# Performance work log

Measured on AMD Instinct MI355X. Metric: run time of the kernel, lower is better.

Reference implementation:

```python
import jax, jax.numpy as jnp
import numpy as np

N, DZ, L, H, MLPH, INC = 256, 256, 256, 512, 2048, 8
CAT_IDX = np.arange(0, 192, 2)                      # 96 categorical token positions (interleaved)
NUM_IDX = np.setdiff1d(np.arange(L), CAT_IDX)       # 160 numerical token positions
CARDS = [4, 16, 128]                                # cardinality per categorical group
GSZ = 32                                            # tokens per categorical group
NUM_CARD = 100                                      # cardinality of quantized numerical params


def setup_inputs() -> dict:
    ks = list(jax.random.split(jax.random.key(0), 24))
    def nrm(shape, s=0.02):
        return jax.random.normal(ks.pop(), shape, jnp.float32) * s
    inp = {}
    inp['z'] = jax.random.normal(ks.pop(), (N, DZ), jnp.float32)
    inp['mlp_w0'] = nrm((DZ, MLPH)); inp['mlp_b0'] = jnp.zeros((MLPH,), jnp.float32)
    inp['mlp_w1'] = nrm((MLPH, MLPH)); inp['mlp_b1'] = jnp.zeros((MLPH,), jnp.float32)
    inp['mlp_w2'] = nrm((MLPH, MLPH)); inp['mlp_b2'] = jnp.zeros((MLPH,), jnp.float32)
    inp['conv_w'] = nrm((H, INC)); inp['conv_b'] = jnp.zeros((H,), jnp.float32)
    for g, card in enumerate(CARDS):
        inp[f'cat_w{g}'] = nrm((H, card)); inp[f'cat_b{g}'] = jnp.zeros((card,), jnp.float32)
    inp['num_w'] = nrm((H, 2)); inp['num_b'] = jnp.zeros((2,), jnp.float32)
    inp['num_target'] = jax.random.uniform(ks.pop(), (N, len(NUM_IDX)), jnp.float32)
    inp['cat_target'] = jax.random.randint(ks.pop(), (N, len(CAT_IDX)), 0, 4, jnp.int32)
    return inp


def reference(z, mlp_w0, mlp_b0, mlp_w1, mlp_b1, mlp_w2, mlp_b2, conv_w, conv_b,
              cat_w0, cat_b0, cat_w1, cat_b1, cat_w2, cat_b2, num_w, num_b,
              num_target, cat_target):
    n = z.shape[0]
    # MLP: fc0 -> act -> fc1 -> act -> fc2
    h = z @ mlp_w0 + mlp_b0
    h = jax.nn.relu(h) @ mlp_w1 + mlp_b1
    h = jax.nn.relu(h) @ mlp_w2 + mlp_b2
    h = h.reshape(n, INC, L)                        # (N, C=8, L)
    # act + 1x1 conv to hidden_size, then transpose -> (N, L, H)
    u = jnp.einsum('ncl,hc->nlh', jax.nn.relu(h), conv_w) + conv_b
    # ---- categorical tokens: gather, per-cardinality heads, CE NLL, argmax sample ----
    hc = u[:, CAT_IDX, :]                           # (N, 96, H)
    heads = [(cat_w0, cat_b0), (cat_w1, cat_b1), (cat_w2, cat_b2)]
    nlls, samps = [], []
    for g, (w, b) in enumerate(heads):
        hg = hc[:, g * GSZ:(g + 1) * GSZ, :]        # (N, 32, H)
        logits = hg @ w + b                         # (N, 32, card)
        logp = jax.nn.log_softmax(logits, axis=-1)
        tg = cat_target[:, g * GSZ:(g + 1) * GSZ]
        nlls.append(-jnp.take_along_axis(logp, tg[..., None], axis=-1)[..., 0])
        samps.append(jnp.argmax(logits, axis=-1))
    cat_nll = jnp.concatenate(nlls, axis=1)         # (N, 96)
    cat_samples = jnp.concatenate(samps, axis=1)    # (N, 96)
    # ---- numerical tokens: gather, 2-param discretized logistic, NLL, mode sample ----
    hn = u[:, NUM_IDX, :]                           # (N, 160, H)
    p = hn @ num_w + num_b                          # (N, 160, 2)
    mu = jax.nn.sigmoid(p[..., 0])
    s = jax.nn.softplus(p[..., 1]) + 1e-4
    hb = 1.0 / (2.0 * (NUM_CARD - 1))               # half bin width
    t = num_target
    cdf_p = jax.nn.sigmoid((t + hb - mu) / s)
    cdf_m = jax.nn.sigmoid((t - hb - mu) / s)
    prob = jnp.where(t < hb, cdf_p, jnp.where(t > 1.0 - hb, 1.0 - cdf_m, cdf_p - cdf_m))
    num_nll = -jnp.log(jnp.maximum(prob, 1e-7))     # (N, 160)
    num_samples = jax.lax.stop_gradient(jnp.round(mu * (NUM_CARD - 1)) / (NUM_CARD - 1))
    # ---- scatter samples back into the preallocated output tensor ----
    u_out = jnp.zeros((n, L, 3), jnp.float32)
    u_out = u_out.at[:, CAT_IDX, 0].set(cat_samples.astype(jnp.float32))
    u_out = u_out.at[:, NUM_IDX, 1].set(num_samples)
    return u_out, cat_nll, num_nll
```

## Files before the change

### kernel.cpp

```cpp
#include <hip/hip_runtime.h>
#include <hip/hip_fp16.h>
#include <math.h>

#define NN   256
#define LL   256
#define HH   512
#define MLPHv 2048
#define INCv 8
#define NCOLS 150

typedef _Float16 f16x8 __attribute__((ext_vector_type(8)));
typedef float    f32x4 __attribute__((ext_vector_type(4)));
typedef unsigned short ushort_t;

__device__ __forceinline__ void split1(float f, ushort_t& h, ushort_t& l)
{
    __half hh = __float2half_rn(f);
    h = __half_as_ushort(hh);
    l = __half_as_ushort(__float2half_rn((f - __half2float(hh)) * 4096.f));
}

typedef __attribute__((address_space(3))) unsigned int lds_u32;
typedef __attribute__((address_space(1))) const unsigned int glb_u32;
__device__ __forceinline__ void gl_lds16(const ushort_t* g, ushort_t* l)
{
    __builtin_amdgcn_global_load_lds((glb_u32*)g, (lds_u32*)l, 16, 0, 0);
}


__global__ __launch_bounds__(256) void prep_all(
    const float* __restrict__ z,
    const float* __restrict__ w0, const float* __restrict__ w1,
    const float* __restrict__ w2,
    const float* __restrict__ cvw, const float* __restrict__ cvb,
    const float* __restrict__ cw0, const float* __restrict__ cb0,
    const float* __restrict__ cw1, const float* __restrict__ cb1,
    const float* __restrict__ cw2, const float* __restrict__ cb2,
    const float* __restrict__ nw,  const float* __restrict__ nbv,
    ushort_t* __restrict__ W0th, ushort_t* __restrict__ W0tl,
    ushort_t* __restrict__ W1th, ushort_t* __restrict__ W1tl,
    ushort_t* __restrict__ W2th, ushort_t* __restrict__ W2tl,
    ushort_t* __restrict__ zh, ushort_t* __restrict__ zl,
    float* __restrict__ Mf, float* __restrict__ beta)
{
    const int bid = blockIdx.x;
    const int tid = threadIdx.x;
    if (bid < 2176) {
        __shared__ ushort_t lh[64 * 65];
        __shared__ ushort_t ll[64 * 65];
        const float* src; ushort_t* dh; ushort_t* dl; int KS32v, t;
        if (bid < 1024)      { src = w1; dh = W1th; dl = W1tl; KS32v = 64; t = bid; }
        else if (bid < 2048) { src = w2; dh = W2th; dl = W2tl; KS32v = 64; t = bid - 1024; }
        else                 { src = w0; dh = W0th; dl = W0tl; KS32v = 8;  t = bid - 2048; }
        const int k0 = (t >> 5) * 64;
        const int n0 = (t & 31) * 64;
        {
            const int r  = tid >> 2;
            const int cb = (tid & 3) * 16;
            const float* p = src + (size_t)(k0 + r) * 2048 + n0 + cb;
            float fv[16];
#pragma unroll
            for (int q = 0; q < 4; ++q) {
                float4 v = *(const float4*)(p + q * 4);
                fv[q * 4 + 0] = v.x; fv[q * 4 + 1] = v.y;
                fv[q * 4 + 2] = v.z; fv[q * 4 + 3] = v.w;
            }
#pragma unroll
            for (int j = 0; j < 16; ++j) {
                ushort_t h, l;
                split1(fv[j], h, l);
                lh[r * 65 + cb + j] = h;
                ll[r * 65 + cb + j] = l;
            }
        }
        __syncthreads();
        {
            const int c  = tid >> 2;
            const int kq = tid & 3;
            ushort_t hb[16], lb[16];
#pragma unroll
            for (int j = 0; j < 16; ++j) {
                hb[j] = lh[(kq * 16 + j) * 65 + c];
                lb[j] = ll[(kq * 16 + j) * 65 + c];
            }
            const int gn  = (n0 + c) >> 4;
            const int l16 = c & 15;
#pragma unroll
            for (int o = 0; o < 2; ++o) {
                const int koct  = (k0 >> 3) + kq * 2 + o;
                const int ks    = koct >> 2, koct3 = koct & 3;
                const size_t off = ((size_t)(gn * KS32v + ks) * 64 + l16 + (koct3 << 4)) * 8;
                uint4 v;
                v.x = (unsigned)hb[o*8+0] | ((unsigned)hb[o*8+1] << 16);
                v.y = (unsigned)hb[o*8+2] | ((unsigned)hb[o*8+3] << 16);
                v.z = (unsigned)hb[o*8+4] | ((unsigned)hb[o*8+5] << 16);
                v.w = (unsigned)hb[o*8+6] | ((unsigned)hb[o*8+7] << 16);
                *(uint4*)&dh[off] = v;
                v.x = (unsigned)lb[o*8+0] | ((unsigned)lb[o*8+1] << 16);
                v.y = (unsigned)lb[o*8+2] | ((unsigned)lb[o*8+3] << 16);
                v.z = (unsigned)lb[o*8+4] | ((unsigned)lb[o*8+5] << 16);
                v.w = (unsigned)lb[o*8+6] | ((unsigned)lb[o*8+7] << 16);
                *(uint4*)&dl[off] = v;
            }
        }
    } else if (bid < 2192) {
        const int idx = (bid - 2176) * 256 + tid;
        const int r = idx >> 4, kq = idx & 15;
        const float* p = z + (size_t)r * 256 + kq * 16;
        float fv[16];
#pragma unroll
        for (int q = 0; q < 4; ++q) {
            float4 v = *(const float4*)(p + q * 4);
            fv[q * 4 + 0] = v.x; fv[q * 4 + 1] = v.y;
            fv[q * 4 + 2] = v.z; fv[q * 4 + 3] = v.w;
        }
        ushort_t hb[16], lb[16];
#pragma unroll
        for (int j = 0; j < 16; ++j) split1(fv[j], hb[j], lb[j]);
        const int gm = r >> 4, l16 = r & 15;
#pragma unroll
        for (int o = 0; o < 2; ++o) {
            const int koct = kq * 2 + o;
            const int ks = koct >> 2, koct3 = koct & 3;
            const size_t off = ((size_t)(gm * 8 + ks) * 64 + l16 + (koct3 << 4)) * 8;
            uint4 v;
            v.x = (unsigned)hb[o*8+0] | ((unsigned)hb[o*8+1] << 16);
            v.y = (unsigned)hb[o*8+2] | ((unsigned)hb[o*8+3] << 16);
            v.z = (unsigned)hb[o*8+4] | ((unsigned)hb[o*8+5] << 16);
            v.w = (unsigned)hb[o*8+6] | ((unsigned)hb[o*8+7] << 16);
            *(uint4*)&zh[off] = v;
            v.x = (unsigned)lb[o*8+0] | ((unsigned)lb[o*8+1] << 16);
            v.y = (unsigned)lb[o*8+2] | ((unsigned)lb[o*8+3] << 16);
            v.z = (unsigned)lb[o*8+4] | ((unsigned)lb[o*8+5] << 16);
            v.w = (unsigned)lb[o*8+6] | ((unsigned)lb[o*8+7] << 16);
            *(uint4*)&zl[off] = v;
        }
    } else {
        const int k = bid - 2192;
        const float* W; const float* B; int off, card;
        if (k < 4)        { W = cw0; B = cb0; off = 0;   card = 4;   }
        else if (k < 20)  { W = cw1; B = cb1; off = 4;   card = 16;  }
        else if (k < 148) { W = cw2; B = cb2; off = 20;  card = 128; }
        else              { W = nw;  B = nbv; off = 148; card = 2;   }
        const int kc = k - off;
        float part[INCv + 1];
#pragma unroll
        for (int c = 0; c <= INCv; ++c) part[c] = 0.f;
#pragma unroll
        for (int it = 0; it < 2; ++it) {
            const int h = tid + it * 256;
            const float wv = W[h * card + kc];
#pragma unroll
            for (int c = 0; c < INCv; ++c) part[c] += cvw[h * INCv + c] * wv;
            part[INCv] += cvb[h] * wv;
        }
        __shared__ float red[INCv + 1][4];
        const int lane = tid & 63, wave = tid >> 6;
#pragma unroll
        for (int c = 0; c <= INCv; ++c) {
            float v = part[c];
#pragma unroll
            for (int o = 32; o >= 1; o >>= 1) v += __shfl_down(v, o, 64);
            if (lane == 0) red[c][wave] = v;
        }
        __syncthreads();
        if (tid <= INCv) {
            const float s = red[tid][0] + red[tid][1] + red[tid][2] + red[tid][3];
            if (tid < INCv) Mf[tid * NCOLS + k] = s;
            else            beta[k] = s + B[kc];
        }
    }
}

template <int OUT>
__global__ __launch_bounds__(512, 4) void gemm_pk(
    const ushort_t* __restrict__ Ah, const ushort_t* __restrict__ Al,
    const ushort_t* __restrict__ Bh, const ushort_t* __restrict__ Bl,
    const float* __restrict__ bias, float* __restrict__ part,
    ushort_t* __restrict__ oH, ushort_t* __restrict__ oL,
    int KS32, int kchunk32, int steps)
{
    __shared__ ushort_t sAh[8192];
    __shared__ ushort_t sAl[8192];
    __shared__ ushort_t sBh[4096];
    __shared__ ushort_t sBl[4096];

    const int tid  = threadIdx.x;
    const int lane = tid & 63, w = tid >> 6;
    const int wr   = w >> 1, wc = w & 1;
    const int bx   = blockIdx.x, by = blockIdx.y, bz = blockIdx.z;
    const int kb0  = bz * kchunk32;

    f32x4 accH[2][2], accC[2][2];
#pragma unroll
    for (int r = 0; r < 2; ++r)
#pragma unroll
        for (int c = 0; c < 2; ++c) {
            accH[r][c] = (f32x4){0.f, 0.f, 0.f, 0.f};
            accC[r][c] = (f32x4){0.f, 0.f, 0.f, 0.f};
        }

    for (int t = 0; t < steps; ++t) {
        const int kb = kb0 + t * 2;
#pragma unroll
        for (int i = 0; i < 2; ++i) {
            const int run = w + i * 8;
            const int g = run >> 1, ks = run & 1;
            const size_t f = ((size_t)(by * 8 + g) * KS32 + kb + ks) * 512 + lane * 8;
            gl_lds16(Ah + f, &sAh[run * 512]);
            gl_lds16(Al + f, &sAl[run * 512]);
        }
        {
            const int g = w >> 1, ks = w & 1;
            const size_t f = ((size_t)(bx * 4 + g) * KS32 + kb + ks) * 512 + lane * 8;
            gl_lds16(Bh + f, &sBh[w * 512]);
            gl_lds16(Bl + f, &sBl[w * 512]);
        }
        __syncthreads();

#pragma unroll
        for (int ks = 0; ks < 2; ++ks) {
            f16x8 aH[2], aL[2], bHf[2], bLf[2];
#pragma unroll
            for (int r = 0; r < 2; ++r) {
                const int off = (((wr * 2 + r) * 2 + ks) * 64 + lane) * 8;
                aH[r] = *(const f16x8*)&sAh[off];
                aL[r] = *(const f16x8*)&sAl[off];
            }
#pragma unroll
            for (int c = 0; c < 2; ++c) {
                const int off = (((wc * 2 + c) * 2 + ks) * 64 + lane) * 8;
                bHf[c] = *(const f16x8*)&sBh[off];
                bLf[c] = *(const f16x8*)&sBl[off];
            }
#pragma unroll
            for (int r = 0; r < 2; ++r)
#pragma unroll
                for (int c = 0; c < 2; ++c) {
                    accH[r][c] = __builtin_amdgcn_mfma_f32_16x16x32_f16(aH[r], bHf[c], accH[r][c], 0, 0, 0);
                    accC[r][c] = __builtin_amdgcn_mfma_f32_16x16x32_f16(aH[r], bLf[c], accC[r][c], 0, 0, 0);
                    accC[r][c] = __builtin_amdgcn_mfma_f32_16x16x32_f16(aL[r], bHf[c], accC[r][c], 0, 0, 0);
                }
        }
        __syncthreads();
    }

    const float inv = 1.f / 4096.f;
#pragma unroll
    for (int r = 0; r < 2; ++r)
#pragma unroll
        for (int c = 0; c < 2; ++c) {
            const int row0 = by * 128 + (wr * 2 + r) * 16 + ((lane >> 4) << 2);
            const int col  = bx * 64  + (wc * 2 + c) * 16 + (lane & 15);
            if (OUT == 0) {
                float* po = part + (size_t)bz * 524288;
#pragma unroll
                for (int e = 0; e < 4; ++e)
                    po[(size_t)(row0 + e) * 2048 + col] = accH[r][c][e] + accC[r][c][e] * inv;
            } else {
                const float vb = bias[col];
                const int gm = (by * 8 + wr * 2 + r);
                const int ks = col >> 5, koct3 = (col >> 3) & 3, j = col & 7;
                const size_t fb = ((size_t)(gm * 64 + ks) * 64) * 8 + (koct3 << 4) * 8 + j;
#pragma unroll
                for (int e = 0; e < 4; ++e) {
                    const float v = fmaxf(accH[r][c][e] + accC[r][c][e] * inv + vb, 0.f);
                    ushort_t h, l;
                    split1(v, h, l);
                    const int l16 = ((lane >> 4) << 2) + e;
                    oH[fb + (size_t)l16 * 8] = h;
                    oL[fb + (size_t)l16 * 8] = l;
                }
            }
        }
}

template <bool PACK>
__global__ __launch_bounds__(256) void reduce_pk(
    const float* __restrict__ part, const float* __restrict__ bias,
    ushort_t* __restrict__ oH, ushort_t* __restrict__ oL, float* __restrict__ oF)
{
    const int b  = blockIdx.x;
    const int ct = b & 15, rg = b >> 4;
    const int e  = threadIdx.x * 4;
    const int row = rg * 8 + (e >> 7);
    const int col = ct * 128 + (e & 127);
    const size_t idx = (size_t)row * 2048 + col;
    float4 s = *(const float4*)&bias[col];
#pragma unroll
    for (int k = 0; k < 4; ++k) {
        const float4 p = *(const float4*)&part[(size_t)k * 524288 + idx];
        s.x += p.x; s.y += p.y; s.z += p.z; s.w += p.w;
    }
    s.x = fmaxf(s.x, 0.f); s.y = fmaxf(s.y, 0.f);
    s.z = fmaxf(s.z, 0.f); s.w = fmaxf(s.w, 0.f);
    if (PACK) {
        ushort_t h[4], l[4];
        split1(s.x, h[0], l[0]); split1(s.y, h[1], l[1]);
        split1(s.z, h[2], l[2]); split1(s.w, h[3], l[3]);
        const int gm = row >> 4, l16 = row & 15;
        const int ks = col >> 5, koct3 = (col >> 3) & 3, j = col & 7;
        const size_t off = ((size_t)(gm * 64 + ks) * 64 + l16 + (koct3 << 4)) * 8 + j;
        ushort4 hv = {h[0], h[1], h[2], h[3]};
        ushort4 lv = {l[0], l[1], l[2], l[3]};
        *(ushort4*)&oH[off] = hv;
        *(ushort4*)&oL[off] = lv;
    } else {
        *(float4*)&oF[idx] = s;
    }
}

__global__ __launch_bounds__(256) void heads_kernel(
    const float* __restrict__ rh, const float* __restrict__ Mf,
    const float* __restrict__ beta, const int* __restrict__ cat_target,
    const float* __restrict__ num_target, float* __restrict__ out)
{
    const int bx  = blockIdx.x;
    const int tid = threadIdx.x;
    __shared__ float Ms[INCv][128];
    __shared__ float Bsh[128];
    if (bx < 96) {
        const int g = bx >> 5;
        const int card = (g == 0) ? 4 : (g == 1) ? 16 : 128;
        const int off  = (g == 0) ? 0 : (g == 1) ? 4  : 20;
        for (int i = tid; i < card * INCv; i += 256) {
            int c = i / card, k = i % card;
            Ms[c][k] = Mf[c * NCOLS + off + k];
        }
        for (int i = tid; i < card; i += 256) Bsh[i] = beta[off + i];
        __syncthreads();

        const int idx = (bx & 31) * 256 + tid;
        const int n = idx >> 5, j = idx & 31;
        const int ci = g * 32 + j;
        const int l  = ci * 2;
        float rv[INCv];
#pragma unroll
        for (int c = 0; c < INCv; ++c) rv[c] = rh[n * MLPHv + c * LL + l];

        float mx = -1e30f; int arg = 0;
        for (int k = 0; k < card; ++k) {
            float s = Bsh[k];
#pragma unroll
            for (int c = 0; c < INCv; ++c) s += rv[c] * Ms[c][k];
            if (s > mx) { mx = s; arg = k; }
        }
        const int tg = cat_target[n * 96 + ci];
        float sum = 0.f, stg = 0.f;
        for (int k = 0; k < card; ++k) {
            float s = Bsh[k];
#pragma unroll
            for (int c = 0; c < INCv; ++c) s += rv[c] * Ms[c][k];
            sum += expf(s - mx);
            if (k == tg) stg = s;
        }
        const float lse = mx + logf(sum);
        out[NN * LL * 3 + n * 96 + ci] = lse - stg;
        float* u = out + (size_t)(n * LL + l) * 3;
        u[0] = (float)arg; u[1] = 0.f; u[2] = 0.f;
    } else {
        const int idx = (bx - 96) * 256 + tid;
        const int n = idx / 160, ni = idx % 160;
        const int l = (ni < 96) ? (2 * ni + 1) : (96 + ni);
        float rv[INCv];
#pragma unroll
        for (int c = 0; c < INCv; ++c) rv[c] = rh[n * MLPHv + c * LL + l];
        float p0 = beta[148], p1 = beta[149];
#pragma unroll
        for (int c = 0; c < INCv; ++c) {
            p0 += rv[c] * Mf[c * NCOLS + 148];
            p1 += rv[c] * Mf[c * NCOLS + 149];
        }
        const float mu = 1.f / (1.f + expf(-p0));
        const float sp = (p1 > 20.f) ? p1 : log1pf(expf(p1));
        const float s  = sp + 1e-4f;
        const float hb = 1.f / 198.f;
        const float t  = num_target[n * 160 + ni];
        const float cp = 1.f / (1.f + expf(-((t + hb - mu) / s)));
        const float cm = 1.f / (1.f + expf(-((t - hb - mu) / s)));
        const float prob = (t < hb) ? cp : ((t > 1.f - hb) ? (1.f - cm) : (cp - cm));
        out[NN * LL * 3 + NN * 96 + n * 160 + ni] = -logf(fmaxf(prob, 1e-7f));
        float* u = out + (size_t)(n * LL + l) * 3;
        u[0] = 0.f; u[1] = rintf(mu * 99.f) / 99.f; u[2] = 0.f;
    }
}

extern "C" void kernel_launch(void* const* d_in, const int* in_sizes, int n_in,
                              void* d_out, int out_size, void* d_ws, size_t ws_size,
                              hipStream_t stream)
{
    const float* z   = (const float*)d_in[0];
    const float* w0  = (const float*)d_in[1];
    const float* b0  = (const float*)d_in[2];
    const float* w1  = (const float*)d_in[3];
    const float* b1  = (const float*)d_in[4];
    const float* w2  = (const float*)d_in[5];
    const float* b2  = (const float*)d_in[6];
    const float* cvw = (const float*)d_in[7];
    const float* cvb = (const float*)d_in[8];
    const float* cw0 = (const float*)d_in[9];
    const float* cb0 = (const float*)d_in[10];
    const float* cw1 = (const float*)d_in[11];
    const float* cb1 = (const float*)d_in[12];
    const float* cw2 = (const float*)d_in[13];
    const float* cb2 = (const float*)d_in[14];
    const float* nw  = (const float*)d_in[15];
    const float* nb  = (const float*)d_in[16];
    const float* num_target = (const float*)d_in[17];
    const int*   cat_target = (const int*)d_in[18];
    float* out = (float*)d_out;
    float* ws  = (float*)d_ws;

    size_t o = 0;
    float*    part = ws + o;                o += 4ull * 524288;
    float*    rh2  = ws + o;                o += 524288;
    float*    Mf   = ws + o;                o += 1536;
    float*    beta = ws + o;                o += 256;
    ushort_t* zh   = (ushort_t*)(ws + o);   o += 32768;
    ushort_t* zl   = (ushort_t*)(ws + o);   o += 32768;
    ushort_t* r0h  = (ushort_t*)(ws + o);   o += 262144;
    ushort_t* r0l  = (ushort_t*)(ws + o);   o += 262144;
    ushort_t* r1h  = (ushort_t*)(ws + o);   o += 262144;
    ushort_t* r1l  = (ushort_t*)(ws + o);   o += 262144;
    ushort_t* W0th = (ushort_t*)(ws + o);   o += 262144;
    ushort_t* W0tl = (ushort_t*)(ws + o);   o += 262144;
    ushort_t* W1th = (ushort_t*)(ws + o);   o += 2097152;
    ushort_t* W1tl = (ushort_t*)(ws + o);   o += 2097152;
    ushort_t* W2th = (ushort_t*)(ws + o);   o += 2097152;
    ushort_t* W2tl = (ushort_t*)(ws + o);   o += 2097152;

    prep_all<<<dim3(2342), 256, 0, stream>>>(
        z, w0, w1, w2, cvw, cvb, cw0, cb0, cw1, cb1, cw2, cb2, nw, nb,
        W0th, W0tl, W1th, W1tl, W2th, W2tl, zh, zl, Mf, beta);

    gemm_pk<1><<<dim3(32, 2, 1), 512, 0, stream>>>(
        zh, zl, W0th, W0tl, b0, nullptr, r0h, r0l, 8, 8, 4);

    gemm_pk<0><<<dim3(32, 2, 4), 512, 0, stream>>>(
        r0h, r0l, W1th, W1tl, nullptr, part, nullptr, nullptr, 64, 16, 8);
    reduce_pk<true><<<dim3(512), 256, 0, stream>>>(part, b1, r1h, r1l, nullptr);

    gemm_pk<0><<<dim3(32, 2, 4), 512, 0, stream>>>(
        r1h, r1l, W2th, W2tl, nullptr, part, nullptr, nullptr, 64, 16, 8);
    reduce_pk<false><<<dim3(512), 256, 0, stream>>>(part, b2, nullptr, nullptr, rh2);

    heads_kernel<<<dim3(256), 256, 0, stream>>>(
        rh2, Mf, beta, cat_target, num_target, out);
}
```

Before: 81.35 us.

## Double-buffer GEMM LDS loads, fuse final split-K reduce into heads, stage fp32 in prep

```diff
diff --git a/kernel.cpp b/kernel.cpp
--- a/kernel.cpp
+++ b/kernel.cpp
@@ -18,6 +18,21 @@
     __half hh = __float2half_rn(f);
     h = __half_as_ushort(hh);
     l = __half_as_ushort(__float2half_rn((f - __half2float(hh)) * 4096.f));
+}
+
+__device__ __forceinline__ void pack8(const float* fv, uint4& hv, uint4& lv)
+{
+    ushort_t h[8], l[8];
+#pragma unroll
+    for (int j = 0; j < 8; ++j) split1(fv[j], h[j], l[j]);
+    hv.x = (unsigned)h[0] | ((unsigned)h[1] << 16);
+    hv.y = (unsigned)h[2] | ((unsigned)h[3] << 16);
+    hv.z = (unsigned)h[4] | ((unsigned)h[5] << 16);
+    hv.w = (unsigned)h[6] | ((unsigned)h[7] << 16);
+    lv.x = (unsigned)l[0] | ((unsigned)l[1] << 16);
+    lv.y = (unsigned)l[2] | ((unsigned)l[3] << 16);
+    lv.z = (unsigned)l[4] | ((unsigned)l[5] << 16);
+    lv.w = (unsigned)l[6] | ((unsigned)l[7] << 16);
 }
 
 typedef __attribute__((address_space(3))) unsigned int lds_u32;
@@ -46,8 +61,7 @@
     const int bid = blockIdx.x;
     const int tid = threadIdx.x;
     if (bid < 2176) {
-        __shared__ ushort_t lh[64 * 65];
-        __shared__ ushort_t ll[64 * 65];
+        __shared__ float lfs[64 * 68];
         const float* src; ushort_t* dh; ushort_t* dl; int KS32v, t;
         if (bid < 1024)      { src = w1; dh = W1th; dl = W1tl; KS32v = 64; t = bid; }
         else if (bid < 2048) { src = w2; dh = W2th; dl = W2tl; KS32v = 64; t = bid - 1024; }
@@ -58,20 +72,9 @@
             const int r  = tid >> 2;
             const int cb = (tid & 3) * 16;
             const float* p = src + (size_t)(k0 + r) * 2048 + n0 + cb;
-            float fv[16];
-#pragma unroll
-            for (int q = 0; q < 4; ++q) {
-                float4 v = *(const float4*)(p + q * 4);
-                fv[q * 4 + 0] = v.x; fv[q * 4 + 1] = v.y;
-                fv[q * 4 + 2] = v.z; fv[q * 4 + 3] = v.w;
-            }
-#pragma unroll
-            for (int j = 0; j < 16; ++j) {
-                ushort_t h, l;
-                split1(fv[j], h, l);
-                lh[r * 65 + cb + j] = h;
-                ll[r * 65 + cb + j] = l;
-            }
+#pragma unroll
+            for (int q = 0; q < 4; ++q)
+                *(float4*)&lfs[r * 68 + cb + q * 4] = *(const float4*)(p + q * 4);
         }
         __syncthreads();
         {
@@ -79,10 +82,8 @@
             const int kq = tid & 3;
             ushort_t hb[16], lb[16];
 #pragma unroll
-            for (int j = 0; j < 16; ++j) {
-                hb[j] = lh[(kq * 16 + j) * 65 + c];
-                lb[j] = ll[(kq * 16 + j) * 65 + c];
-            }
+            for (int j = 0; j < 16; ++j)
+                split1(lfs[(kq * 16 + j) * 68 + c], hb[j], lb[j]);
             const int gn  = (n0 + c) >> 4;
             const int l16 = c & 15;
 #pragma unroll
@@ -180,10 +181,10 @@
     ushort_t* __restrict__ oH, ushort_t* __restrict__ oL,
     int KS32, int kchunk32, int steps)
 {
-    __shared__ ushort_t sAh[8192];
-    __shared__ ushort_t sAl[8192];
-    __shared__ ushort_t sBh[4096];
-    __shared__ ushort_t sBl[4096];
+    __shared__ ushort_t sAh[2][8192];
+    __shared__ ushort_t sAl[2][8192];
+    __shared__ ushort_t sBh[2][4096];
+    __shared__ ushort_t sBl[2][4096];
 
     const int tid  = threadIdx.x;
     const int lane = tid & 63, w = tid >> 6;
@@ -200,23 +201,45 @@
             accC[r][c] = (f32x4){0.f, 0.f, 0.f, 0.f};
         }
 
-    for (int t = 0; t < steps; ++t) {
-        const int kb = kb0 + t * 2;
+    {
+        const int kb = kb0;
 #pragma unroll
         for (int i = 0; i < 2; ++i) {
             const int run = w + i * 8;
             const int g = run >> 1, ks = run & 1;
             const size_t f = ((size_t)(by * 8 + g) * KS32 + kb + ks) * 512 + lane * 8;
-            gl_lds16(Ah + f, &sAh[run * 512]);
-            gl_lds16(Al + f, &sAl[run * 512]);
-        }
-        {
+            gl_lds16(Ah + f, &sAh[0][run * 512]);
+            gl_lds16(Al + f, &sAl[0][run * 512]);
+        }
+        const int g = w >> 1, ks = w & 1;
+        const size_t f = ((size_t)(bx * 4 + g) * KS32 + kb + ks) * 512 + lane * 8;
+        gl_lds16(Bh + f, &sBh[0][w * 512]);
+        gl_lds16(Bl + f, &sBl[0][w * 512]);
+    }
+
+    for (int t = 0; t < steps; ++t) {
+        const int cur = t & 1;
+        const int nxt = t + 1;
+        if (nxt < steps) {
+            const int kb = kb0 + nxt * 2;
+            const int nb = nxt & 1;
+#pragma unroll
+            for (int i = 0; i < 2; ++i) {
+                const int run = w + i * 8;
+                const int g = run >> 1, ks = run & 1;
+                const size_t f = ((size_t)(by * 8 + g) * KS32 + kb + ks) * 512 + lane * 8;
+                gl_lds16(Ah + f, &sAh[nb][run * 512]);
+                gl_lds16(Al + f, &sAl[nb][run * 512]);
+            }
             const int g = w >> 1, ks = w & 1;
             const size_t f = ((size_t)(bx * 4 + g) * KS32 + kb + ks) * 512 + lane * 8;
-            gl_lds16(Bh + f, &sBh[w * 512]);
-            gl_lds16(Bl + f, &sBl[w * 512]);
-        }
-        __syncthreads();
+            gl_lds16(Bh + f, &sBh[nb][w * 512]);
+            gl_lds16(Bl + f, &sBl[nb][w * 512]);
+            asm volatile("s_waitcnt vmcnt(6)" ::: "memory");
+        } else {
+            asm volatile("s_waitcnt vmcnt(0)" ::: "memory");
+        }
+        __builtin_amdgcn_s_barrier();
 
 #pragma unroll
         for (int ks = 0; ks < 2; ++ks) {
@@ -224,14 +247,14 @@
 #pragma unroll
             for (int r = 0; r < 2; ++r) {
                 const int off = (((wr * 2 + r) * 2 + ks) * 64 + lane) * 8;
-                aH[r] = *(const f16x8*)&sAh[off];
-                aL[r] = *(const f16x8*)&sAl[off];
+                aH[r] = *(const f16x8*)&sAh[cur][off];
+                aL[r] = *(const f16x8*)&sAl[cur][off];
             }
 #pragma unroll
             for (int c = 0; c < 2; ++c) {
                 const int off = (((wc * 2 + c) * 2 + ks) * 64 + lane) * 8;
-                bHf[c] = *(const f16x8*)&sBh[off];
-                bLf[c] = *(const f16x8*)&sBl[off];
+                bHf[c] = *(const f16x8*)&sBh[cur][off];
+                bLf[c] = *(const f16x8*)&sBl[cur][off];
             }
 #pragma unroll
             for (int r = 0; r < 2; ++r)
@@ -242,7 +265,7 @@
                     accC[r][c] = __builtin_amdgcn_mfma_f32_16x16x32_f16(aL[r], bHf[c], accC[r][c], 0, 0, 0);
                 }
         }
-        __syncthreads();
+        __builtin_amdgcn_s_barrier();
     }
 
     const float inv = 1.f / 4096.f;
@@ -275,10 +298,9 @@
         }
 }
 
-template <bool PACK>
 __global__ __launch_bounds__(256) void reduce_pk(
     const float* __restrict__ part, const float* __restrict__ bias,
-    ushort_t* __restrict__ oH, ushort_t* __restrict__ oL, float* __restrict__ oF)
+    ushort_t* __restrict__ oH, ushort_t* __restrict__ oL)
 {
     const int b  = blockIdx.x;
     const int ct = b & 15, rg = b >> 4;
@@ -294,26 +316,23 @@
     }
     s.x = fmaxf(s.x, 0.f); s.y = fmaxf(s.y, 0.f);
     s.z = fmaxf(s.z, 0.f); s.w = fmaxf(s.w, 0.f);
-    if (PACK) {
-        ushort_t h[4], l[4];
-        split1(s.x, h[0], l[0]); split1(s.y, h[1], l[1]);
-        split1(s.z, h[2], l[2]); split1(s.w, h[3], l[3]);
-        const int gm = row >> 4, l16 = row & 15;
-        const int ks = col >> 5, koct3 = (col >> 3) & 3, j = col & 7;
-        const size_t off = ((size_t)(gm * 64 + ks) * 64 + l16 + (koct3 << 4)) * 8 + j;
-        ushort4 hv = {h[0], h[1], h[2], h[3]};
-        ushort4 lv = {l[0], l[1], l[2], l[3]};
-        *(ushort4*)&oH[off] = hv;
-        *(ushort4*)&oL[off] = lv;
-    } else {
-        *(float4*)&oF[idx] = s;
-    }
+    ushort_t h[4], l[4];
+    split1(s.x, h[0], l[0]); split1(s.y, h[1], l[1]);
+    split1(s.z, h[2], l[2]); split1(s.w, h[3], l[3]);
+    const int gm = row >> 4, l16 = row & 15;
+    const int ks = col >> 5, koct3 = (col >> 3) & 3, j = col & 7;
+    const size_t off = ((size_t)(gm * 64 + ks) * 64 + l16 + (koct3 << 4)) * 8 + j;
+    ushort4 hv = {h[0], h[1], h[2], h[3]};
+    ushort4 lv = {l[0], l[1], l[2], l[3]};
+    *(ushort4*)&oH[off] = hv;
+    *(ushort4*)&oL[off] = lv;
 }
 
 __global__ __launch_bounds__(256) void heads_kernel(
-    const float* __restrict__ rh, const float* __restrict__ Mf,
-    const float* __restrict__ beta, const int* __restrict__ cat_target,
-    const float* __restrict__ num_target, float* __restrict__ out)
+    const float* __restrict__ part, const float* __restrict__ b2,
+    const float* __restrict__ Mf, const float* __restrict__ beta,
+    const int* __restrict__ cat_target, const float* __restrict__ num_target,
+    float* __restrict__ out)
 {
     const int bx  = blockIdx.x;
     const int tid = threadIdx.x;
@@ -336,7 +355,13 @@
         const int l  = ci * 2;
         float rv[INCv];
 #pragma unroll
-        for (int c = 0; c < INCv; ++c) rv[c] = rh[n * MLPHv + c * LL + l];
+        for (int c = 0; c < INCv; ++c) {
+            const size_t e = (size_t)n * MLPHv + c * LL + l;
+            float s = b2[c * LL + l];
+#pragma unroll
+            for (int k = 0; k < 4; ++k) s += part[(size_t)k * 524288 + e];
+            rv[c] = fmaxf(s, 0.f);
+        }
 
         float mx = -1e30f; int arg = 0;
         for (int k = 0; k < card; ++k) {
@@ -364,7 +389,13 @@
         const int l = (ni < 96) ? (2 * ni + 1) : (96 + ni);
         float rv[INCv];
 #pragma unroll
-        for (int c = 0; c < INCv; ++c) rv[c] = rh[n * MLPHv + c * LL + l];
+        for (int c = 0; c < INCv; ++c) {
+            const size_t e = (size_t)n * MLPHv + c * LL + l;
+            float s = b2[c * LL + l];
+#pragma unroll
+            for (int k = 0; k < 4; ++k) s += part[(size_t)k * 524288 + e];
+            rv[c] = fmaxf(s, 0.f);
+        }
         float p0 = beta[148], p1 = beta[149];
 #pragma unroll
         for (int c = 0; c < INCv; ++c) {
@@ -413,7 +444,6 @@
 
     size_t o = 0;
     float*    part = ws + o;                o += 4ull * 524288;
-    float*    rh2  = ws + o;                o += 524288;
     float*    Mf   = ws + o;                o += 1536;
     float*    beta = ws + o;                o += 256;
     ushort_t* zh   = (ushort_t*)(ws + o);   o += 32768;
@@ -438,12 +468,11 @@
 
     gemm_pk<0><<<dim3(32, 2, 4), 512, 0, stream>>>(
         r0h, r0l, W1th, W1tl, nullptr, part, nullptr, nullptr, 64, 16, 8);
-    reduce_pk<true><<<dim3(512), 256, 0, stream>>>(part, b1, r1h, r1l, nullptr);
+    reduce_pk<<<dim3(512), 256, 0, stream>>>(part, b1, r1h, r1l);
 
     gemm_pk<0><<<dim3(32, 2, 4), 512, 0, stream>>>(
         r1h, r1l, W2th, W2tl, nullptr, part, nullptr, nullptr, 64, 16, 8);
-    reduce_pk<false><<<dim3(512), 256, 0, stream>>>(part, b2, nullptr, nullptr, rh2);
 
     heads_kernel<<<dim3(256), 256, 0, stream>>>(
-        rh2, Mf, beta, cat_target, num_target, out);
-}
+        part, b2, Mf, beta, cat_target, num_target, out);
+}
```

Measured after the change: 77.81 us. 4.3% less time.
